# Optimization experiments

Hardware: AMD Instinct MI355X
Metric: run time of the kernel (lower is better)

Reference implementation:

```python
import jax, jax.numpy as jnp
import numpy as np

N = 50000
E = 1_600_000
F_IN = 128
HID = 64
OUT = 2
NEG_SLOPE = 0.2  # PyG GATConv default


def setup_inputs() -> dict:
    key = jax.random.key(0)
    ks = jax.random.split(key, 10)
    x = jax.random.normal(ks[0], (N, F_IN), jnp.float32)
    edge_index = jax.random.randint(ks[1], (2, E), 0, N, dtype=jnp.int32)
    # glorot-ish scaled params
    W1 = jax.random.normal(ks[2], (F_IN, HID), jnp.float32) / np.sqrt(F_IN)
    a1_src = jax.random.normal(ks[3], (HID,), jnp.float32) / np.sqrt(HID)
    a1_dst = jax.random.normal(ks[4], (HID,), jnp.float32) / np.sqrt(HID)
    b1 = jnp.zeros((HID,), jnp.float32)
    W2 = jax.random.normal(ks[5], (HID, OUT), jnp.float32) / np.sqrt(HID)
    a2_src = jax.random.normal(ks[6], (OUT,), jnp.float32) / np.sqrt(OUT)
    a2_dst = jax.random.normal(ks[7], (OUT,), jnp.float32) / np.sqrt(OUT)
    b2 = jnp.zeros((OUT,), jnp.float32)
    return {"x": x, "edge_index": edge_index, "W1": W1, "a1_src": a1_src,
            "a1_dst": a1_dst, "b1": b1, "W2": W2, "a2_src": a2_src,
            "a2_dst": a2_dst, "b2": b2}


def gat_layer(x, edge_index, W, a_src, a_dst, b):
    n = x.shape[0]
    loop = jnp.arange(n, dtype=edge_index.dtype)
    src = jnp.concatenate([edge_index[0], loop])  # [E+N] message sources j
    dst = jnp.concatenate([edge_index[1], loop])  # [E+N] message targets i
    h = x @ W                                     # [N, out]
    alpha_s = h @ a_src                           # [N]
    alpha_d = h @ a_dst                           # [N]
    e = jax.nn.leaky_relu(alpha_s[src] + alpha_d[dst], NEG_SLOPE)  # [E+N]
    # segment softmax over edges sharing the same destination node
    emax = jax.ops.segment_max(e, dst, num_segments=n)
    ee = jnp.exp(e - emax[dst])
    denom = jax.ops.segment_sum(ee, dst, num_segments=n)
    alpha = ee / denom[dst]
    out = jax.ops.segment_sum(alpha[:, None] * h[src], dst, num_segments=n)
    return out + b


def reference(x, edge_index, W1, a1_src, a1_dst, b1, W2, a2_src, a2_dst, b2):
    h = gat_layer(x, edge_index, W1, a1_src, a1_dst, b1)
    h = jax.nn.relu(h)
    # dropout(p=0.5) is identity in eval mode
    return gat_layer(h, edge_index, W2, a2_src, a2_dst, b2)
```

## Files before the change

### kernel.cpp

```cpp
#include <hip/hip_runtime.h>
#include <hip/hip_fp16.h>
#include <math.h>


#define NEG 0.2f
#define NEGINF (-1e30f)

#define BPW   128
#define NB    391
#define BLKS  192
#define SCAP  64
#define CAPB  4864

__device__ __forceinline__ float leaky(float v) { return v >= 0.f ? v : NEG * v; }

__global__ __launch_bounds__(256) void k_bucket(
    const int* __restrict__ esrc, const int* __restrict__ edst, int E,
    int* __restrict__ slabs, int* __restrict__ slabcnt) {
    __shared__ int cnt[NB];
    int t = threadIdx.x, blk = blockIdx.x;
    for (int i = t; i < NB; i += 256) cnt[i] = 0;
    __syncthreads();
    int chunk = (E + BLKS - 1) / BLKS;
    int lo = blk * chunk, hi = min(E, lo + chunk);
    for (int e = lo + t; e < hi; e += 256) {
        int s = esrc[e], d = edst[e];
        int b = d >> 7;
        int pos = atomicAdd(&cnt[b], 1);
        if (pos < SCAP)
            slabs[((size_t)b * BLKS + blk) * SCAP + pos] = s | ((d & 127) << 16);
    }
    __syncthreads();
    for (int i = t; i < NB; i += 256)
        slabcnt[i * BLKS + blk] = min(cnt[i], SCAP);
}

__global__ __launch_bounds__(256) void k_gemm(
    const float* __restrict__ x, const float* __restrict__ W1,
    const float* __restrict__ a1s_, const float* __restrict__ a1d_, int N,
    __half* __restrict__ h1h, float* __restrict__ as1, float* __restrict__ ad1) {
    __shared__ float xs[64][129];
    __shared__ float red[2][4][64];
    int t = threadIdx.x;
    int r0 = blockIdx.x * 64;
    {
        const float4* xg = (const float4*)x;
        for (int j = 0; j < 8; j++) {
            int idx = t + j * 256;
            int row = idx >> 5, c4 = idx & 31;
            float4 v = make_float4(0.f, 0.f, 0.f, 0.f);
            if (r0 + row < N) v = xg[(size_t)(r0 + row) * 32 + c4];
            *(float4*)&xs[row][c4 * 4] = v;
        }
    }
    __syncthreads();
    int lane = t & 63;
    int wid = __builtin_amdgcn_readfirstlane(t >> 6);
    const float* Wp = W1 + 16 * wid;
    float acc[16];
#pragma unroll
    for (int j = 0; j < 16; j++) acc[j] = 0.f;
#pragma unroll 4
    for (int k4 = 0; k4 < 32; k4++) {
        float4 xv = *(const float4*)&xs[lane][k4 * 4];
#pragma unroll
        for (int kk = 0; kk < 4; kk++) {
            const float* wrow = Wp + (k4 * 4 + kk) * 64;
            float xk = (kk == 0) ? xv.x : (kk == 1) ? xv.y : (kk == 2) ? xv.z : xv.w;
#pragma unroll
            for (int j = 0; j < 16; j++) acc[j] = fmaf(xk, wrow[j], acc[j]);
        }
    }
    int row = r0 + lane;
    float ps = 0.f, pd = 0.f;
#pragma unroll
    for (int j = 0; j < 16; j++) {
        ps = fmaf(acc[j], a1s_[16 * wid + j], ps);
        pd = fmaf(acc[j], a1d_[16 * wid + j], pd);
    }
    red[0][wid][lane] = ps;
    red[1][wid][lane] = pd;
    if (row < N) {
        unsigned int pk[8];
#pragma unroll
        for (int j = 0; j < 8; j++) {
            __half2 h2 = __floats2half2_rn(acc[2 * j], acc[2 * j + 1]);
            pk[j] = *(unsigned int*)&h2;
        }
        __half* dst = h1h + (size_t)row * 64 + 16 * wid;
        ((int4*)dst)[0] = make_int4(pk[0], pk[1], pk[2], pk[3]);
        ((int4*)dst)[1] = make_int4(pk[4], pk[5], pk[6], pk[7]);
    }
    __syncthreads();
    if (t < 64) {
        int r = r0 + t;
        if (r < N) as1[r] = red[0][0][t] + red[0][1][t] + red[0][2][t] + red[0][3][t];
    } else if (t < 128) {
        int t2 = t - 64, r = r0 + t2;
        if (r < N) ad1[r] = red[1][0][t2] + red[1][1][t2] + red[1][2][t2] + red[1][3][t2];
    }
}

__global__ __launch_bounds__(256) void k_sortb(
    const int* __restrict__ slabs, const int* __restrict__ slabcnt, int N,
    int* __restrict__ ssrc32, int* __restrict__ nodebase,
    int* __restrict__ nodedeg) {
    __shared__ int cstage[CAPB];
    __shared__ unsigned short outs[CAPB];
    __shared__ int ccnt[BLKS];
    __shared__ int coff[BLKS];
    __shared__ int hist[BPW], pexcl[BPW], cur[BPW];
    __shared__ int ctotS, btotS;
    int b = blockIdx.x, t = threadIdx.x;

    for (int i = t; i < BLKS; i += 256) ccnt[i] = slabcnt[b * BLKS + i];
    for (int i = t; i < BPW; i += 256) hist[i] = 0;
    __syncthreads();

    if (t < 64) {
        int carry = 0;
        for (int c0 = 0; c0 < BLKS; c0 += 64) {
            int v = ccnt[c0 + t];
            int incl = v;
            for (int off = 1; off < 64; off <<= 1) {
                int u = __shfl_up(incl, off, 64);
                if (t >= off) incl += u;
            }
            coff[c0 + t] = carry + incl - v;
            carry += __shfl(incl, 63, 64);
        }
        if (t == 0) ctotS = carry;
    }
    __syncthreads();
    int ctot = min(ctotS, CAPB);

    for (int c = t; c < BLKS; c += 256) {
        int cn = ccnt[c], off = coff[c];
        const int* cell = slabs + ((size_t)b * BLKS + c) * SCAP;
        for (int j = 0; j < cn; j++) {
            int p = off + j;
            if (p < CAPB) cstage[p] = cell[j];
        }
    }
    __syncthreads();

    for (int i = t; i < ctot; i += 256) atomicAdd(&hist[cstage[i] >> 16], 1);
    __syncthreads();

    if (t < 64) {
        int h0 = hist[2 * t], h1v = hist[2 * t + 1];
        int p0 = (h0 + 3) & ~3, p1 = (h1v + 3) & ~3;
        int ps = p0 + p1, incl = ps;
        for (int off = 1; off < 64; off <<= 1) {
            int u = __shfl_up(incl, off, 64);
            if (t >= off) incl += u;
        }
        int ex = incl - ps;
        pexcl[2 * t] = ex;          cur[2 * t] = ex;
        pexcl[2 * t + 1] = ex + p0; cur[2 * t + 1] = ex + p0;
        if (t == 63) btotS = incl;
    }
    __syncthreads();

    for (int i = t; i < ctot; i += 256) {
        int en = cstage[i];
        int p = atomicAdd(&cur[en >> 16], 1);
        if (p < CAPB) outs[p] = (unsigned short)(en & 0xFFFF);
    }
    __syncthreads();

    int v0 = b * BPW;
    for (int i = t; i < BPW; i += 256) {
        int h = hist[i], ph = (h + 3) & ~3;
        for (int j = h; j < ph; j++) {
            int pos = pexcl[i] + j;
            if (pos < CAPB) outs[pos] = (unsigned short)(v0 + i);
        }
    }
    __syncthreads();

    int btot = min(btotS, CAPB);
    int* dst = ssrc32 + (size_t)b * CAPB;
    for (int i = t; i < btot; i += 256) dst[i] = (int)outs[i];

    for (int i = t; i < BPW; i += 256) {
        int v = v0 + i;
        if (v < N) { nodebase[v] = b * CAPB + pexcl[i]; nodedeg[v] = hist[i]; }
    }
}

__global__ __launch_bounds__(256) void k_agg1f(
    const __half* __restrict__ h1h, const float* __restrict__ as1,
    const float* __restrict__ ad1, const int* __restrict__ nodebase,
    const int* __restrict__ nodedeg, const int* __restrict__ ssrc32,
    const float* __restrict__ b1, const float* __restrict__ W2,
    const float* __restrict__ a2s, const float* __restrict__ a2d, int N,
    float4* __restrict__ node4) {
    __shared__ __align__(16) float pw[4][128];
    int lane = threadIdx.x & 63;
    int wid = __builtin_amdgcn_readfirstlane(threadIdx.x >> 6);
    int i = blockIdx.x * 4 + wid;
    if (i >= N) return;
    float ad_i = ad1[i];
    int base = nodebase[i], deg = nodedeg[i];

    float e0 = NEGINF, e1 = NEGINF;
    if (lane < deg)      e0 = leaky(as1[ssrc32[base + lane]] + ad_i);
    if (lane + 64 < deg) e1 = leaky(as1[ssrc32[base + lane + 64]] + ad_i);
    float ml = fmaxf(e0, e1), sl = 0.f;
    for (int t = base + lane + 128; t < base + deg; t += 64) {
        float e = leaky(as1[ssrc32[t]] + ad_i);
        float mN = fmaxf(ml, e);
        sl = sl * __expf(ml - mN) + __expf(e - mN);
        ml = mN;
    }
    sl += __expf(e0 - ml) + __expf(e1 - ml);
    for (int off = 32; off > 0; off >>= 1) {
        float m2 = __shfl_xor(ml, off, 64);
        float s2 = __shfl_xor(sl, off, 64);
        float mN = fmaxf(ml, m2);
        sl = sl * __expf(ml - mN) + s2 * __expf(m2 - mN);
        ml = mN;
    }
    float e_self = leaky(as1[i] + ad_i);
    float m = fmaxf(ml, e_self);
    float s = sl * __expf(ml - m) + __expf(e_self - m);
    float inv_s = 1.f / s;

    pw[wid][lane]      = (lane < deg)      ? __expf(e0 - m) * inv_s : 0.f;
    pw[wid][lane + 64] = (lane + 64 < deg) ? __expf(e1 - m) * inv_s : 0.f;

    int nq = (min(deg, 128) + 3) >> 2;
    const int4* sq = (const int4*)(ssrc32 + base);
    float acc = __expf(e_self - m) * inv_s * __half2float(h1h[(size_t)i * 64 + lane]);
#pragma unroll 2
    for (int q = 0; q < nq; ++q) {
        int4 s4 = sq[q];
        float4 p4 = *(const float4*)&pw[wid][q * 4];
        float g0 = __half2float(h1h[(size_t)s4.x * 64 + lane]);
        float g1 = __half2float(h1h[(size_t)s4.y * 64 + lane]);
        float g2 = __half2float(h1h[(size_t)s4.z * 64 + lane]);
        float g3 = __half2float(h1h[(size_t)s4.w * 64 + lane]);
        acc = fmaf(p4.x, g0, acc);
        acc = fmaf(p4.y, g1, acc);
        acc = fmaf(p4.z, g2, acc);
        acc = fmaf(p4.w, g3, acc);
    }
    for (int t = base + 128; t < base + deg; ++t) {
        int sv = ssrc32[t];
        float p = __expf(leaky(as1[sv] + ad_i) - m) * inv_s;
        acc = fmaf(p, __half2float(h1h[(size_t)sv * 64 + lane]), acc);
    }

    float hr = fmaxf(acc + b1[lane], 0.f);
    float2 w2 = ((const float2*)W2)[lane];
    float t0 = hr * w2.x, t1 = hr * w2.y;
    for (int mm = 32; mm > 0; mm >>= 1) {
        t0 += __shfl_xor(t0, mm, 64);
        t1 += __shfl_xor(t1, mm, 64);
    }
    if (lane == 0) {
        float s0 = t0 * a2s[0] + t1 * a2s[1];
        float d0 = t0 * a2d[0] + t1 * a2d[1];
        node4[i] = make_float4(t0, t1, s0, d0);
    }
}

__global__ __launch_bounds__(256) void k_agg2(
    const float4* __restrict__ node4, const int* __restrict__ nodebase,
    const int* __restrict__ nodedeg, const int* __restrict__ ssrc32,
    const float* __restrict__ b2, int N, float2* __restrict__ out) {
    int lane = threadIdx.x & 63, wid = threadIdx.x >> 6;
    int i = blockIdx.x * 4 + wid;
    if (i >= N) return;
    float4 ni = node4[i];
    float adi = ni.w;
    int base = nodebase[i], end = base + nodedeg[i];
    float ml = NEGINF, sl = 0.f, A0 = 0.f, A1 = 0.f;
    for (int t = base + lane; t < end; t += 64) {
        float4 nd = node4[ssrc32[t]];
        float e = leaky(nd.z + adi);
        float mN = fmaxf(ml, e);
        float c1 = __expf(ml - mN), p = __expf(e - mN);
        sl = fmaf(sl, c1, p);
        A0 = fmaf(A0, c1, p * nd.x);
        A1 = fmaf(A1, c1, p * nd.y);
        ml = mN;
    }
    for (int off = 32; off > 0; off >>= 1) {
        float m2 = __shfl_xor(ml, off, 64);
        float s2 = __shfl_xor(sl, off, 64);
        float a02 = __shfl_xor(A0, off, 64);
        float a12 = __shfl_xor(A1, off, 64);
        float mN = fmaxf(ml, m2);
        float c1 = __expf(ml - mN), c2 = __expf(m2 - mN);
        sl = sl * c1 + s2 * c2;
        A0 = A0 * c1 + a02 * c2;
        A1 = A1 * c1 + a12 * c2;
        ml = mN;
    }
    float e_self = leaky(ni.z + adi);
    float mN = fmaxf(ml, e_self);
    float c1 = __expf(ml - mN), c2 = __expf(e_self - mN);
    float s = sl * c1 + c2;
    float a0 = A0 * c1 + c2 * ni.x;
    float a1 = A1 * c1 + c2 * ni.y;
    if (lane == 0) out[i] = make_float2(a0 / s + b2[0], a1 / s + b2[1]);
}

extern "C" void kernel_launch(void* const* d_in, const int* in_sizes, int n_in,
                              void* d_out, int out_size, void* d_ws, size_t ws_size,
                              hipStream_t stream) {
    const float* x   = (const float*)d_in[0];
    const int*   ei  = (const int*)d_in[1];
    const float* W1  = (const float*)d_in[2];
    const float* a1s = (const float*)d_in[3];
    const float* a1d = (const float*)d_in[4];
    const float* b1  = (const float*)d_in[5];
    const float* W2  = (const float*)d_in[6];
    const float* a2s = (const float*)d_in[7];
    const float* a2d = (const float*)d_in[8];
    const float* b2  = (const float*)d_in[9];

    int N = in_sizes[0] / 128;
    int E = in_sizes[1] / 2;
    const int* esrc = ei;
    const int* edst = ei + E;

    __half* h1h   = (__half*)d_ws;
    float*  as1   = (float*)(h1h + (size_t)N * 64);
    float*  ad1   = as1 + N;
    float*  pad0  = ad1 + N;
    float4* node4 = (float4*)(pad0 + N);
    int* slabs    = (int*)(node4 + N);
    int* slabcnt  = slabs + (size_t)NB * BLKS * SCAP;
    int* ssrc32   = slabcnt + (size_t)NB * BLKS;
    int* nodebase = ssrc32 + (size_t)NB * CAPB;
    int* nodedeg  = nodebase + N;

    k_bucket<<<BLKS, 256, 0, stream>>>(esrc, edst, E, slabs, slabcnt);
    k_gemm<<<(N + 63) / 64, 256, 0, stream>>>(x, W1, a1s, a1d, N, h1h, as1, ad1);
    k_sortb<<<NB, 256, 0, stream>>>(slabs, slabcnt, N, ssrc32, nodebase, nodedeg);
    k_agg1f<<<(N + 3) / 4, 256, 0, stream>>>(h1h, as1, ad1, nodebase, nodedeg,
                                             ssrc32, b1, W2, a2s, a2d, N, node4);
    k_agg2<<<(N + 3) / 4, 256, 0, stream>>>(node4, nodebase, nodedeg, ssrc32, b2,
                                            N, (float2*)d_out);
}
```

Before: 201.9 us.

## Fuse bucket sort and layer-1 GEMM into one heterogeneous launch, widen bucketing

The separate GEMM and per-bucket sort kernels are merged into one launch. The first 391 blocks do the sort and the rest compute x@W1 plus the attention scalars, sharing LDS through a union. Bucketing now uses 256 blocks of 1024 threads with a smaller slab capacity of 48, and the GEMM uses 512 threads with 8 columns per wave. This removes a launch and lets sort and GEMM work run at the same time on the GPU. In exchange, the smaller per-cell capacity raises the risk that edges are dropped when a cell overflows, and the larger union LDS footprint may lower occupancy.

```diff
diff --git a/kernel.cpp b/kernel.cpp
--- a/kernel.cpp
+++ b/kernel.cpp
@@ -8,184 +8,189 @@
 
 #define BPW   128
 #define NB    391
-#define BLKS  192
-#define SCAP  64
+#define NBB   256
+#define SCAP  48
 #define CAPB  4864
+#define SB    391
 
 __device__ __forceinline__ float leaky(float v) { return v >= 0.f ? v : NEG * v; }
 
-__global__ __launch_bounds__(256) void k_bucket(
+__global__ __launch_bounds__(1024) void k_bucket(
     const int* __restrict__ esrc, const int* __restrict__ edst, int E,
     int* __restrict__ slabs, int* __restrict__ slabcnt) {
     __shared__ int cnt[NB];
     int t = threadIdx.x, blk = blockIdx.x;
-    for (int i = t; i < NB; i += 256) cnt[i] = 0;
+    for (int i = t; i < NB; i += 1024) cnt[i] = 0;
     __syncthreads();
-    int chunk = (E + BLKS - 1) / BLKS;
+    int chunk = (E + NBB - 1) / NBB;
     int lo = blk * chunk, hi = min(E, lo + chunk);
-    for (int e = lo + t; e < hi; e += 256) {
+    for (int e = lo + t; e < hi; e += 1024) {
         int s = esrc[e], d = edst[e];
         int b = d >> 7;
         int pos = atomicAdd(&cnt[b], 1);
         if (pos < SCAP)
-            slabs[((size_t)b * BLKS + blk) * SCAP + pos] = s | ((d & 127) << 16);
+            slabs[((size_t)b * NBB + blk) * SCAP + pos] = s | ((d & 127) << 16);
     }
     __syncthreads();
-    for (int i = t; i < NB; i += 256)
-        slabcnt[i * BLKS + blk] = min(cnt[i], SCAP);
-}
-
-__global__ __launch_bounds__(256) void k_gemm(
+    for (int i = t; i < NB; i += 1024)
+        slabcnt[i * NBB + blk] = min(cnt[i], SCAP);
+}
+
+union SmemU {
+    struct { float xs[64][129]; float red[2][8][64]; } g;
+    struct {
+        int cstage[CAPB]; unsigned short outs[CAPB];
+        int ccnt[NBB]; int coff[NBB];
+        int hist[BPW]; int pexcl[BPW]; int cur[BPW];
+        int ctotS; int btotS;
+    } s;
+};
+
+__global__ __launch_bounds__(512) void k_sortgemm(
+    const int* __restrict__ slabs, const int* __restrict__ slabcnt,
     const float* __restrict__ x, const float* __restrict__ W1,
     const float* __restrict__ a1s_, const float* __restrict__ a1d_, int N,
-    __half* __restrict__ h1h, float* __restrict__ as1, float* __restrict__ ad1) {
-    __shared__ float xs[64][129];
-    __shared__ float red[2][4][64];
+    int* __restrict__ ssrc32, int* __restrict__ nodebase,
+    int* __restrict__ nodedeg, __half* __restrict__ h1h,
+    float* __restrict__ as1, float* __restrict__ ad1) {
+    __shared__ SmemU u;
     int t = threadIdx.x;
-    int r0 = blockIdx.x * 64;
-    {
-        const float4* xg = (const float4*)x;
+    if ((int)blockIdx.x < SB) {
+        int b = blockIdx.x;
+        for (int i = t; i < NBB; i += 512) u.s.ccnt[i] = slabcnt[b * NBB + i];
+        for (int i = t; i < BPW; i += 512) u.s.hist[i] = 0;
+        __syncthreads();
+        if (t < 64) {
+            int carry = 0;
+            for (int c0 = 0; c0 < NBB; c0 += 64) {
+                int v = u.s.ccnt[c0 + t];
+                int incl = v;
+                for (int off = 1; off < 64; off <<= 1) {
+                    int uu = __shfl_up(incl, off, 64);
+                    if (t >= off) incl += uu;
+                }
+                u.s.coff[c0 + t] = carry + incl - v;
+                carry += __shfl(incl, 63, 64);
+            }
+            if (t == 0) u.s.ctotS = carry;
+        }
+        __syncthreads();
+        int ctot = min(u.s.ctotS, CAPB);
+        for (int c = t; c < NBB; c += 512) {
+            int cn = u.s.ccnt[c], off = u.s.coff[c];
+            const int* cell = slabs + ((size_t)b * NBB + c) * SCAP;
+            for (int j = 0; j < cn; j++) {
+                int p = off + j;
+                if (p < CAPB) u.s.cstage[p] = cell[j];
+            }
+        }
+        __syncthreads();
+        for (int i = t; i < ctot; i += 512) atomicAdd(&u.s.hist[u.s.cstage[i] >> 16], 1);
+        __syncthreads();
+        if (t < 64) {
+            int h0 = u.s.hist[2 * t], h1v = u.s.hist[2 * t + 1];
+            int p0 = (h0 + 3) & ~3, p1 = (h1v + 3) & ~3;
+            int ps = p0 + p1, incl = ps;
+            for (int off = 1; off < 64; off <<= 1) {
+                int uu = __shfl_up(incl, off, 64);
+                if (t >= off) incl += uu;
+            }
+            int ex = incl - ps;
+            u.s.pexcl[2 * t] = ex;          u.s.cur[2 * t] = ex;
+            u.s.pexcl[2 * t + 1] = ex + p0; u.s.cur[2 * t + 1] = ex + p0;
+            if (t == 63) u.s.btotS = incl;
+        }
+        __syncthreads();
+        for (int i = t; i < ctot; i += 512) {
+            int en = u.s.cstage[i];
+            int p = atomicAdd(&u.s.cur[en >> 16], 1);
+            if (p < CAPB) u.s.outs[p] = (unsigned short)(en & 0xFFFF);
+        }
+        __syncthreads();
+        int v0 = b * BPW;
+        for (int i = t; i < BPW; i += 512) {
+            int h = u.s.hist[i], ph = (h + 3) & ~3;
+            for (int j = h; j < ph; j++) {
+                int pos = u.s.pexcl[i] + j;
+                if (pos < CAPB) u.s.outs[pos] = (unsigned short)(v0 + i);
+            }
+        }
+        __syncthreads();
+        int btot = min(u.s.btotS, CAPB);
+        int* dst = ssrc32 + (size_t)b * CAPB;
+        for (int i = t; i < btot; i += 512) dst[i] = (int)u.s.outs[i];
+        for (int i = t; i < BPW; i += 512) {
+            int v = v0 + i;
+            if (v < N) { nodebase[v] = b * CAPB + u.s.pexcl[i]; nodedeg[v] = u.s.hist[i]; }
+        }
+    } else {
+        int gb = blockIdx.x - SB;
+        int r0 = gb * 64;
+        {
+            const float4* xg = (const float4*)x;
+            for (int j = 0; j < 4; j++) {
+                int idx = t + j * 512;
+                int row = idx >> 5, c4 = idx & 31;
+                float4 v = make_float4(0.f, 0.f, 0.f, 0.f);
+                if (r0 + row < N) v = xg[(size_t)(r0 + row) * 32 + c4];
+                *(float4*)&u.g.xs[row][c4 * 4] = v;
+            }
+        }
+        __syncthreads();
+        int lane = t & 63;
+        int w = __builtin_amdgcn_readfirstlane(t >> 6);
+        const float* Wp = W1 + 8 * w;
+        float acc[8];
+#pragma unroll
+        for (int j = 0; j < 8; j++) acc[j] = 0.f;
+#pragma unroll 4
+        for (int k4 = 0; k4 < 32; k4++) {
+            float4 xv = *(const float4*)&u.g.xs[lane][k4 * 4];
+#pragma unroll
+            for (int kk = 0; kk < 4; kk++) {
+                const float* wrow = Wp + (k4 * 4 + kk) * 64;
+                float xk = (kk == 0) ? xv.x : (kk == 1) ? xv.y : (kk == 2) ? xv.z : xv.w;
+#pragma unroll
+                for (int j = 0; j < 8; j++) acc[j] = fmaf(xk, wrow[j], acc[j]);
+            }
+        }
+        int row = r0 + lane;
+        float ps = 0.f, pd = 0.f;
+#pragma unroll
         for (int j = 0; j < 8; j++) {
-            int idx = t + j * 256;
-            int row = idx >> 5, c4 = idx & 31;
-            float4 v = make_float4(0.f, 0.f, 0.f, 0.f);
-            if (r0 + row < N) v = xg[(size_t)(r0 + row) * 32 + c4];
-            *(float4*)&xs[row][c4 * 4] = v;
-        }
-    }
-    __syncthreads();
-    int lane = t & 63;
-    int wid = __builtin_amdgcn_readfirstlane(t >> 6);
-    const float* Wp = W1 + 16 * wid;
-    float acc[16];
-#pragma unroll
-    for (int j = 0; j < 16; j++) acc[j] = 0.f;
-#pragma unroll 4
-    for (int k4 = 0; k4 < 32; k4++) {
-        float4 xv = *(const float4*)&xs[lane][k4 * 4];
-#pragma unroll
-        for (int kk = 0; kk < 4; kk++) {
-            const float* wrow = Wp + (k4 * 4 + kk) * 64;
-            float xk = (kk == 0) ? xv.x : (kk == 1) ? xv.y : (kk == 2) ? xv.z : xv.w;
-#pragma unroll
-            for (int j = 0; j < 16; j++) acc[j] = fmaf(xk, wrow[j], acc[j]);
-        }
-    }
-    int row = r0 + lane;
-    float ps = 0.f, pd = 0.f;
-#pragma unroll
-    for (int j = 0; j < 16; j++) {
-        ps = fmaf(acc[j], a1s_[16 * wid + j], ps);
-        pd = fmaf(acc[j], a1d_[16 * wid + j], pd);
-    }
-    red[0][wid][lane] = ps;
-    red[1][wid][lane] = pd;
-    if (row < N) {
-        unsigned int pk[8];
-#pragma unroll
-        for (int j = 0; j < 8; j++) {
-            __half2 h2 = __floats2half2_rn(acc[2 * j], acc[2 * j + 1]);
-            pk[j] = *(unsigned int*)&h2;
-        }
-        __half* dst = h1h + (size_t)row * 64 + 16 * wid;
-        ((int4*)dst)[0] = make_int4(pk[0], pk[1], pk[2], pk[3]);
-        ((int4*)dst)[1] = make_int4(pk[4], pk[5], pk[6], pk[7]);
-    }
-    __syncthreads();
-    if (t < 64) {
-        int r = r0 + t;
-        if (r < N) as1[r] = red[0][0][t] + red[0][1][t] + red[0][2][t] + red[0][3][t];
-    } else if (t < 128) {
-        int t2 = t - 64, r = r0 + t2;
-        if (r < N) ad1[r] = red[1][0][t2] + red[1][1][t2] + red[1][2][t2] + red[1][3][t2];
-    }
-}
-
-__global__ __launch_bounds__(256) void k_sortb(
-    const int* __restrict__ slabs, const int* __restrict__ slabcnt, int N,
-    int* __restrict__ ssrc32, int* __restrict__ nodebase,
-    int* __restrict__ nodedeg) {
-    __shared__ int cstage[CAPB];
-    __shared__ unsigned short outs[CAPB];
-    __shared__ int ccnt[BLKS];
-    __shared__ int coff[BLKS];
-    __shared__ int hist[BPW], pexcl[BPW], cur[BPW];
-    __shared__ int ctotS, btotS;
-    int b = blockIdx.x, t = threadIdx.x;
-
-    for (int i = t; i < BLKS; i += 256) ccnt[i] = slabcnt[b * BLKS + i];
-    for (int i = t; i < BPW; i += 256) hist[i] = 0;
-    __syncthreads();
-
-    if (t < 64) {
-        int carry = 0;
-        for (int c0 = 0; c0 < BLKS; c0 += 64) {
-            int v = ccnt[c0 + t];
-            int incl = v;
-            for (int off = 1; off < 64; off <<= 1) {
-                int u = __shfl_up(incl, off, 64);
-                if (t >= off) incl += u;
-            }
-            coff[c0 + t] = carry + incl - v;
-            carry += __shfl(incl, 63, 64);
-        }
-        if (t == 0) ctotS = carry;
-    }
-    __syncthreads();
-    int ctot = min(ctotS, CAPB);
-
-    for (int c = t; c < BLKS; c += 256) {
-        int cn = ccnt[c], off = coff[c];
-        const int* cell = slabs + ((size_t)b * BLKS + c) * SCAP;
-        for (int j = 0; j < cn; j++) {
-            int p = off + j;
-            if (p < CAPB) cstage[p] = cell[j];
-        }
-    }
-    __syncthreads();
-
-    for (int i = t; i < ctot; i += 256) atomicAdd(&hist[cstage[i] >> 16], 1);
-    __syncthreads();
-
-    if (t < 64) {
-        int h0 = hist[2 * t], h1v = hist[2 * t + 1];
-        int p0 = (h0 + 3) & ~3, p1 = (h1v + 3) & ~3;
-        int ps = p0 + p1, incl = ps;
-        for (int off = 1; off < 64; off <<= 1) {
-            int u = __shfl_up(incl, off, 64);
-            if (t >= off) incl += u;
-        }
-        int ex = incl - ps;
-        pexcl[2 * t] = ex;          cur[2 * t] = ex;
-        pexcl[2 * t + 1] = ex + p0; cur[2 * t + 1] = ex + p0;
-        if (t == 63) btotS = incl;
-    }
-    __syncthreads();
-
-    for (int i = t; i < ctot; i += 256) {
-        int en = cstage[i];
-        int p = atomicAdd(&cur[en >> 16], 1);
-        if (p < CAPB) outs[p] = (unsigned short)(en & 0xFFFF);
-    }
-    __syncthreads();
-
-    int v0 = b * BPW;
-    for (int i = t; i < BPW; i += 256) {
-        int h = hist[i], ph = (h + 3) & ~3;
-        for (int j = h; j < ph; j++) {
-            int pos = pexcl[i] + j;
-            if (pos < CAPB) outs[pos] = (unsigned short)(v0 + i);
-        }
-    }
-    __syncthreads();
-
-    int btot = min(btotS, CAPB);
-    int* dst = ssrc32 + (size_t)b * CAPB;
-    for (int i = t; i < btot; i += 256) dst[i] = (int)outs[i];
-
-    for (int i = t; i < BPW; i += 256) {
-        int v = v0 + i;
-        if (v < N) { nodebase[v] = b * CAPB + pexcl[i]; nodedeg[v] = hist[i]; }
+            ps = fmaf(acc[j], a1s_[8 * w + j], ps);
+            pd = fmaf(acc[j], a1d_[8 * w + j], pd);
+        }
+        u.g.red[0][w][lane] = ps;
+        u.g.red[1][w][lane] = pd;
+        if (row < N) {
+            unsigned int pk[4];
+#pragma unroll
+            for (int j = 0; j < 4; j++) {
+                __half2 h2 = __floats2half2_rn(acc[2 * j], acc[2 * j + 1]);
+                pk[j] = *(unsigned int*)&h2;
+            }
+            *(int4*)(h1h + (size_t)row * 64 + 8 * w) =
+                make_int4(pk[0], pk[1], pk[2], pk[3]);
+        }
+        __syncthreads();
+        if (t < 64) {
+            int r = r0 + t;
+            if (r < N) {
+                float s = 0.f;
+#pragma unroll
+                for (int ww = 0; ww < 8; ww++) s += u.g.red[0][ww][t];
+                as1[r] = s;
+            }
+        } else if (t < 128) {
+            int t2 = t - 64, r = r0 + t2;
+            if (r < N) {
+                float s = 0.f;
+#pragma unroll
+                for (int ww = 0; ww < 8; ww++) s += u.g.red[1][ww][t2];
+                ad1[r] = s;
+            }
+        }
     }
 }
 
@@ -333,14 +338,15 @@
     float*  pad0  = ad1 + N;
     float4* node4 = (float4*)(pad0 + N);
     int* slabs    = (int*)(node4 + N);
-    int* slabcnt  = slabs + (size_t)NB * BLKS * SCAP;
-    int* ssrc32   = slabcnt + (size_t)NB * BLKS;
+    int* slabcnt  = slabs + (size_t)NB * NBB * SCAP;
+    int* ssrc32   = slabcnt + (size_t)NB * NBB;
     int* nodebase = ssrc32 + (size_t)NB * CAPB;
     int* nodedeg  = nodebase + N;
 
-    k_bucket<<<BLKS, 256, 0, stream>>>(esrc, edst, E, slabs, slabcnt);
-    k_gemm<<<(N + 63) / 64, 256, 0, stream>>>(x, W1, a1s, a1d, N, h1h, as1, ad1);
-    k_sortb<<<NB, 256, 0, stream>>>(slabs, slabcnt, N, ssrc32, nodebase, nodedeg);
+    int nbG = (N + 63) / 64;
+    k_bucket<<<NBB, 1024, 0, stream>>>(esrc, edst, E, slabs, slabcnt);
+    k_sortgemm<<<SB + nbG, 512, 0, stream>>>(slabs, slabcnt, x, W1, a1s, a1d, N,
+                                             ssrc32, nodebase, nodedeg, h1h, as1, ad1);
     k_agg1f<<<(N + 3) / 4, 256, 0, stream>>>(h1h, as1, ad1, nodebase, nodedeg,
                                              ssrc32, b1, W2, a2s, a2d, N, node4);
     k_agg2<<<(N + 3) / 4, 256, 0, stream>>>(node4, nodebase, nodedeg, ssrc32, b2,
```

Measured after the change: 180.0 us. 10.8% less time.
